# Optimization experiments

Hardware: AMD Instinct MI355X
Metric: run time of the kernel (lower is better)

Reference implementation:

```python
import jax, jax.numpy as jnp
import numpy as np

NUM_HEADS = 16
ROPE_BASE = 10000.0


def _rope_cos_sin(T, head_dim, dtype):
    # standard rotary: angles[t, i] = t * base^(-2i/head_dim), half-split layout
    inv_freq = 1.0 / (ROPE_BASE ** (jnp.arange(0, head_dim, 2, dtype=jnp.float32) / head_dim))
    ang = jnp.arange(T, dtype=jnp.float32)[:, None] * inv_freq[None, :]  # [T, hd/2]
    cos = jnp.concatenate([jnp.cos(ang), jnp.cos(ang)], axis=-1).astype(dtype)  # [T, hd]
    sin = jnp.concatenate([jnp.sin(ang), jnp.sin(ang)], axis=-1).astype(dtype)
    return cos, sin


def _rotate_half(t):
    t1, t2 = jnp.split(t, 2, axis=-1)
    return jnp.concatenate([-t2, t1], axis=-1)


def _apply_rope(t, cos, sin):
    # t: [B, H, T, hd]; cos/sin: [T, hd]
    return t * cos[None, None] + _rotate_half(t) * sin[None, None]


def setup_inputs() -> dict:
    key = jax.random.key(0)
    B, T, C = 2, 2048, 1024
    k1, k2, k3 = jax.random.split(key, 3)
    x = jax.random.normal(k1, (B, T, C), dtype=jnp.float32)
    w_attn = jax.random.normal(k2, (C, 3 * C), dtype=jnp.float32) * (C ** -0.5)
    w_proj = jax.random.normal(k3, (C, C), dtype=jnp.float32) * (C ** -0.5)
    return {"x": x, "w_attn": w_attn, "w_proj": w_proj}


def reference(x, w_attn, w_proj):
    B, T, C = x.shape
    H = NUM_HEADS
    hd = C // H

    qkv = x @ w_attn  # [B, T, 3C]
    q, k, v = jnp.split(qkv, 3, axis=-1)
    # [B, T, C] -> [B, H, T, hd]
    q = q.reshape(B, T, H, hd).transpose(0, 2, 1, 3)
    k = k.reshape(B, T, H, hd).transpose(0, 2, 1, 3)
    v = v.reshape(B, T, H, hd).transpose(0, 2, 1, 3)

    cos, sin = _rope_cos_sin(T, hd, x.dtype)
    q = _apply_rope(q, cos, sin)
    k = _apply_rope(k, cos, sin)

    scale = 1.0 / np.sqrt(hd).astype(np.float32)
    att = jnp.einsum('bhqd,bhkd->bhqk', q, k) * scale  # [B, H, T, T]
    causal = jnp.tril(jnp.ones((T, T), dtype=bool))
    att = jnp.where(causal[None, None], att, jnp.array(-jnp.inf, dtype=att.dtype))
    att = jax.nn.softmax(att, axis=-1)
    y = jnp.einsum('bhqk,bhkd->bhqd', att, v)  # [B, H, T, hd]
    y = y.transpose(0, 2, 1, 3).reshape(B, T, C)
    return y @ w_proj
```

## Files before the change

kernel.cpp:

```cpp
#include <hip/hip_runtime.h>

typedef unsigned short u16;
typedef unsigned int u32;
typedef unsigned long long u64;
typedef __attribute__((ext_vector_type(8))) short s16x8;
typedef __attribute__((ext_vector_type(8))) __bf16 bf16x8;
typedef __attribute__((ext_vector_type(4))) float fx4;
typedef __attribute__((ext_vector_type(16))) float fx16;
typedef __attribute__((ext_vector_type(2))) u32 u32x2;
typedef __attribute__((ext_vector_type(4))) u32 u32x4;

__device__ __forceinline__ fx4 mfma_16x16x32(s16x8 a, s16x8 b, fx4 c) {
  return __builtin_amdgcn_mfma_f32_16x16x32_bf16(
      __builtin_bit_cast(bf16x8, a), __builtin_bit_cast(bf16x8, b), c, 0, 0, 0);
}
__device__ __forceinline__ fx16 mfma_32x32x16(s16x8 a, s16x8 b, fx16 c) {
  return __builtin_amdgcn_mfma_f32_32x32x16_bf16(
      __builtin_bit_cast(bf16x8, a), __builtin_bit_cast(bf16x8, b), c, 0, 0, 0);
}

__device__ __forceinline__ u16 f2bf(float f) {
  u32 u = __builtin_bit_cast(u32, f);
  u32 r = u + 0x7fffu + ((u >> 16) & 1u);
  return (u16)(r >> 16);
}
__device__ __forceinline__ float bf2f(u16 h) {
  u32 u = ((u32)h) << 16;
  return __builtin_bit_cast(float, u);
}

__device__ __forceinline__ u32 cvtpk(float lo, float hi) {
  u32 r;
  asm("v_cvt_pk_bf16_f32 %0, %1, %2" : "=v"(r) : "v"(lo), "v"(hi));
  return r;
}

__device__ __forceinline__ float max3f(float a, float b, float c) {
  float r;
  asm("v_max3_f32 %0, %1, %2, %3" : "=v"(r) : "v"(a), "v"(b), "v"(c));
  return r;
}

__device__ __forceinline__ void plswap(u32& x, u32& y) {
  typedef __attribute__((ext_vector_type(2))) unsigned int uix2;
  uix2 r = __builtin_amdgcn_permlane32_swap(x, y, false, false);
  x = r[0];
  y = r[1];
}

__device__ __forceinline__ float xhalf_max(float v) {
  u32 a = __builtin_bit_cast(u32, v), b = a;
  plswap(a, b);
  return fmaxf(__builtin_bit_cast(float, a), __builtin_bit_cast(float, b));
}
__device__ __forceinline__ float xhalf_sum(float v) {
  u32 a = __builtin_bit_cast(u32, v), b = a;
  plswap(a, b);
  return __builtin_bit_cast(float, a) + __builtin_bit_cast(float, b);
}

__device__ __forceinline__ void gload16(const void* g, void* l) {
  __builtin_amdgcn_global_load_lds(
      (const __attribute__((address_space(1))) u32*)g,
      (__attribute__((address_space(3))) u32*)l, 16, 0, 0);
}

#define B_ 2
#define T_ 2048
#define C_ 1024
#define H_ 16
#define HD_ 64
#define BH_ 32
#define M_ 4096
#define CF_ 0.18033688011112042f

__global__ void rope_table_k(float* __restrict__ ct, float* __restrict__ st) {
  int id = blockIdx.x * 256 + threadIdx.x;
  int t = id >> 5, i = id & 31;
  float f = exp2f(-(float)i * (13.287712379549449f / 32.0f));
  float a = (float)t * f;
  float s, c;
  sincosf(a, &s, &c);
  ct[id] = c;
  st[id] = s;
}

__global__ void cvt_f32_bf16_k(const float* __restrict__ in, u16* __restrict__ outp) {
  int id = blockIdx.x * 256 + threadIdx.x;
  const fx4* p = (const fx4*)(in + (u64)id * 8);
  fx4 v0 = p[0], v1 = p[1];
  s16x8 r;
#pragma unroll
  for (int j = 0; j < 4; ++j) {
    r[j] = (short)f2bf(v0[j]);
    r[4 + j] = (short)f2bf(v1[j]);
  }
  *((s16x8*)outp + id) = r;
}

__global__ void transpose_w_k(const float* __restrict__ W, u16* __restrict__ WT,
                              int Ncols, int R) {
  __shared__ u16 T_s[64 * 72];
  int c0 = blockIdx.x * 64, r0 = blockIdx.y * 64;
  int tid = threadIdx.x;
#pragma unroll
  for (int it = 0; it < 4; ++it) {
    int idx = it * 256 + tid;
    int r = idx >> 4, c4 = (idx & 15) * 4;
    fx4 v = *(const fx4*)(W + (u64)(r0 + r) * Ncols + c0 + c4);
#pragma unroll
    for (int j = 0; j < 4; ++j) T_s[(c4 + j) * 72 + r] = f2bf(v[j]);
  }
  __syncthreads();
#pragma unroll
  for (int it = 0; it < 2; ++it) {
    int idx = it * 256 + tid;
    int rc = idx >> 3, c8 = (idx & 7) * 8;
    s16x8 v = *(const s16x8*)(T_s + rc * 72 + c8);
    *(s16x8*)(WT + (u64)(c0 + rc) * R + r0 + c8) = v;
  }
}

template <int EPI>
__global__ __launch_bounds__(256, 4) void gemm_bt_k(
    const u16* __restrict__ A, const u16* __restrict__ B, float* __restrict__ C,
    u16* __restrict__ Qo, u16* __restrict__ Ko, u16* __restrict__ Vo,
    const float* __restrict__ ct, const float* __restrict__ st,
    int M, int N, int K) {
  __shared__ u16 As[128 * 32];
  __shared__ u16 Bs[128 * 32];
  int tid = threadIdx.x, lane = tid & 63, w = tid >> 6;
  int wm = w >> 1, wn = w & 1, l15 = lane & 15, l4 = lane >> 4;
  int nwg = gridDim.x * gridDim.y;
  int id = blockIdx.y * gridDim.x + blockIdx.x;
  int qq = nwg >> 3;
  id = (id & 7) * qq + (id >> 3);
  int m0 = (id / gridDim.x) * 128, n0 = (id % gridDim.x) * 128;
  fx4 acc[4][4] = {};
  int arow = tid >> 2, ac8 = (tid & 3) * 8;
  const u16* Ab = A + (u64)(m0 + arow) * K + ac8;
  const u16* Bb = B + (u64)(n0 + arow) * K + ac8;
  char* AsB = (char*)As + tid * 16;
  char* BsB = (char*)Bs + tid * 16;

  for (int k0 = 0; k0 < K; k0 += 32) {
    __syncthreads();
    gload16(Ab + k0, AsB);
    gload16(Ab + (u64)64 * K + k0, AsB + 4096);
    gload16(Bb + k0, BsB);
    gload16(Bb + (u64)64 * K + k0, BsB + 4096);
    __syncthreads();
    s16x8 a[4], b[4];
#pragma unroll
    for (int mi = 0; mi < 4; ++mi)
      a[mi] = *(const s16x8*)((const char*)As + (wm * 64 + mi * 16 + l15) * 64 + l4 * 16);
#pragma unroll
    for (int ni = 0; ni < 4; ++ni)
      b[ni] = *(const s16x8*)((const char*)Bs + (wn * 64 + ni * 16 + l15) * 64 + l4 * 16);
#pragma unroll
    for (int mi = 0; mi < 4; ++mi)
#pragma unroll
      for (int ni = 0; ni < 4; ++ni)
        acc[mi][ni] = mfma_16x16x32(a[mi], b[ni], acc[mi][ni]);
  }

  if (EPI == 0) {
#pragma unroll
    for (int mi = 0; mi < 4; ++mi)
#pragma unroll
      for (int ni = 0; ni < 4; ++ni)
#pragma unroll
        for (int r = 0; r < 4; ++r) {
          u64 row = (u64)(m0 + wm * 64 + mi * 16 + l4 * 4 + r);
          int col = n0 + wn * 64 + ni * 16 + l15;
          C[row * N + col] = acc[mi][ni][r];
        }
  } else {
#pragma unroll
    for (int mi = 0; mi < 4; ++mi)
#pragma unroll
      for (int r = 0; r < 4; ++r) {
        int row = m0 + wm * 64 + mi * 16 + l4 * 4 + r;
        int b2 = row >> 11, t = row & (T_ - 1);
#pragma unroll
        for (int ni = 0; ni < 2; ++ni) {
          int col = n0 + wn * 64 + ni * 16 + l15;
          int qi = col >> 10, h = (col >> 6) & 15, d = ni * 16 + l15;
          float lo = acc[mi][ni][r], hi = acc[mi][ni + 2][r];
          if (qi == 2) {
            u64 vbase =
                ((((u64)(b2 * H_ + h)) * (T_ / 8) + (t >> 3)) * HD_ + d) * 8 + (t & 7);
            Vo[vbase] = f2bf(lo);
            Vo[vbase + 32 * 8] = f2bf(hi);
          } else {
            float c = ct[t * 32 + d], s = st[t * 32 + d];
            float sc = (qi == 0) ? CF_ : 1.0f;
            u16* dst = (qi == 0) ? Qo : Ko;
            u64 base = ((((u64)(b2 * H_ + h)) * 8 + (d >> 3)) * T_ + t) * 8 + (d & 7);
            dst[base] = f2bf((lo * c - hi * s) * sc);
            dst[base + (u64)4 * T_ * 8] = f2bf((hi * c + lo * s) * sc);
          }
        }
      }
  }
}


#define LOADK(KC, KVI)                                                 \
  do {                                                                 \
    _Pragma("unroll")                                                  \
    for (int ks_ = 0; ks_ < 4; ++ks_)                                  \
      KC[ks_] = *(const s16x8*)(kp[ks_] + (u64)(KVI) * 256);           \
  } while (0)

#define LOADV(VC, KVI)                                                 \
  do {                                                                 \
    const u16* vk_ = vpb + (u64)(KVI) * 2048;                          \
    VC[0] = *(const s16x8*)(vk_);                                      \
    VC[1] = *(const s16x8*)(vk_ + 256);                                \
    VC[2] = *(const s16x8*)(vk_ + 1024);                               \
    VC[3] = *(const s16x8*)(vk_ + 1280);                               \
  } while (0)

#define ATTN_STEP(KC, VC, KVI)                                                \
  do {                                                                        \
    fx16 s_ = {};                                                             \
    __builtin_amdgcn_s_setprio(1);                                            \
    _Pragma("unroll")                                                         \
    for (int ks_ = 0; ks_ < 4; ++ks_)                                         \
      s_ = mfma_32x32x16(KC[ks_], qf[ks_], s_);                               \
    __builtin_amdgcn_s_setprio(0);                                            \
    if ((KVI) == jt) {                                                        \
      _Pragma("unroll")                                                       \
      for (int r_ = 0; r_ < 16; ++r_) {                                       \
        int cr_ = (r_ & 3) + 8 * (r_ >> 2) + 4 * h;                           \
        s_[r_] = (cr_ > ql) ? -1e30f : s_[r_];                                \
      }                                                                       \
    }                                                                         \
    float u0_ = max3f(s_[0], s_[1], s_[2]);                                   \
    float u1_ = max3f(s_[3], s_[4], s_[5]);                                   \
    float u2_ = max3f(s_[6], s_[7], s_[8]);                                   \
    float u3_ = max3f(s_[9], s_[10], s_[11]);                                 \
    float u4_ = max3f(s_[12], s_[13], s_[14]);                                \
    float v0_ = max3f(u0_, u1_, s_[15]);                                      \
    float v1_ = max3f(u2_, u3_, u4_);                                         \
    float rowmax_ = xhalf_max(fmaxf(v0_, v1_));                               \
    if (!__all(rowmax_ <= m + 8.f)) {                                         \
      float mnew_ = fmaxf(m, rowmax_);                                        \
      float corr_ = exp2f(m - mnew_);                                         \
      l *= corr_;                                                             \
      oL *= corr_;                                                            \
      oH *= corr_;                                                            \
      m = mnew_;                                                              \
    }                                                                         \
    float p_[16];                                                             \
    _Pragma("unroll")                                                         \
    for (int r_ = 0; r_ < 16; ++r_) p_[r_] = exp2f(s_[r_] - m);               \
    float a0_ = (p_[0] + p_[8]) + (p_[1] + p_[9]);                            \
    float a1_ = (p_[2] + p_[10]) + (p_[3] + p_[11]);                          \
    float a2_ = (p_[4] + p_[12]) + (p_[5] + p_[13]);                          \
    float a3_ = (p_[6] + p_[14]) + (p_[7] + p_[15]);                          \
    l += xhalf_sum((a0_ + a1_) + (a2_ + a3_));                                \
    u32 x0_ = cvtpk(p_[0], p_[1]), x1_ = cvtpk(p_[2], p_[3]);                 \
    u32 y0_ = cvtpk(p_[4], p_[5]), y1_ = cvtpk(p_[6], p_[7]);                 \
    plswap(x0_, y0_);                                                         \
    plswap(x1_, y1_);                                                         \
    u32x4 f0w_ = {x0_, x1_, y0_, y1_};                                        \
    u32 x2_ = cvtpk(p_[8], p_[9]), x3_ = cvtpk(p_[10], p_[11]);               \
    u32 y2_ = cvtpk(p_[12], p_[13]), y3_ = cvtpk(p_[14], p_[15]);             \
    plswap(x2_, y2_);                                                         \
    plswap(x3_, y3_);                                                         \
    u32x4 f1w_ = {x2_, x3_, y2_, y3_};                                        \
    s16x8 pf0_ = __builtin_bit_cast(s16x8, f0w_);                             \
    s16x8 pf1_ = __builtin_bit_cast(s16x8, f1w_);                             \
    __builtin_amdgcn_s_setprio(1);                                            \
    oL = mfma_32x32x16(VC[0], pf0_, oL);                                      \
    oH = mfma_32x32x16(VC[1], pf0_, oH);                                      \
    oL = mfma_32x32x16(VC[2], pf1_, oL);                                      \
    oH = mfma_32x32x16(VC[3], pf1_, oH);                                      \
    __builtin_amdgcn_s_setprio(0);                                            \
  } while (0)

#define OSTRIDE 68

__global__ __launch_bounds__(256, 3) void attn_fwd_k(
    const u16* __restrict__ Qp, const u16* __restrict__ Kp,
    const u16* __restrict__ Vp, u16* __restrict__ Y) {
  __shared__ float Ob[4 * 32 * OSTRIDE];
  __shared__ float Ml[4 * 32 * 2];
  int tid = threadIdx.x, lane = tid & 63, w = tid >> 6;
  int ql = lane & 31, h = lane >> 5;
  int bh = blockIdx.x & 31;
  int jt = 63 - (blockIdx.x >> 5);
  int q0 = jt * 32;
  int b2 = bh >> 4, head = bh & 15;
  int n = jt + 1;
  int lo = (w * n) >> 2, hi = ((w + 1) * n) >> 2;

  s16x8 qf[4];
#pragma unroll
  for (int ks = 0; ks < 4; ++ks)
    qf[ks] = *(const s16x8*)(Qp + (((u64)bh * 8 + ks * 2 + h) * T_ + q0 + ql) * 8);

  const u16* kp[4];
#pragma unroll
  for (int ks = 0; ks < 4; ++ks)
    kp[ks] = Kp + (((u64)bh * 8 + ks * 2 + h) * T_ + ql) * 8;
  const u16* vpb = Vp + (((u64)bh * (T_ / 8) + h) * HD_ + ql) * 8;

  fx16 oL = {}, oH = {};
  float m = -1e30f, l = 0.f;

  if (lo < hi) {
    s16x8 kA[4], vA[4], kB[4], vB[4];
    LOADK(kA, lo);
    LOADV(vA, lo);
    int kv = lo;
    for (; kv + 1 < hi; kv += 2) {
      LOADK(kB, kv + 1);
      LOADV(vB, kv + 1);
      ATTN_STEP(kA, vA, kv);
      if (kv + 2 < hi) {
        LOADK(kA, kv + 2);
        LOADV(vA, kv + 2);
      }
      ATTN_STEP(kB, vB, kv + 1);
    }
    if (kv < hi) ATTN_STEP(kA, vA, kv);
  }

  {
    float* ob = Ob + (w * 32 + ql) * OSTRIDE;
#pragma unroll
    for (int g = 0; g < 4; ++g) {
      fx4 a = {oL[4 * g], oL[4 * g + 1], oL[4 * g + 2], oL[4 * g + 3]};
      *(fx4*)(ob + 8 * g + 4 * h) = a;
      fx4 b = {oH[4 * g], oH[4 * g + 1], oH[4 * g + 2], oH[4 * g + 3]};
      *(fx4*)(ob + 32 + 8 * g + 4 * h) = b;
    }
    if (h == 0) {
      Ml[(w * 32 + ql) * 2] = m;
      Ml[(w * 32 + ql) * 2 + 1] = l;
    }
  }
  __syncthreads();

  {
    int q = tid >> 3, db = tid & 7;
    float mm0 = Ml[(0 * 32 + q) * 2], ll0 = Ml[(0 * 32 + q) * 2 + 1];
    float mm1 = Ml[(1 * 32 + q) * 2], ll1 = Ml[(1 * 32 + q) * 2 + 1];
    float mm2 = Ml[(2 * 32 + q) * 2], ll2 = Ml[(2 * 32 + q) * 2 + 1];
    float mm3 = Ml[(3 * 32 + q) * 2], ll3 = Ml[(3 * 32 + q) * 2 + 1];
    float mo = fmaxf(fmaxf(mm0, mm1), fmaxf(mm2, mm3));
    float w0 = exp2f(mm0 - mo), w1 = exp2f(mm1 - mo);
    float w2 = exp2f(mm2 - mo), w3 = exp2f(mm3 - mo);
    float rl = 1.0f / (ll0 * w0 + ll1 * w1 + ll2 * w2 + ll3 * w3);
    w0 *= rl; w1 *= rl; w2 *= rl; w3 *= rl;
    const float* ob = Ob + q * OSTRIDE + db * 8;
    fx4 aa = {}, bb = {};
#pragma unroll
    for (int i = 0; i < 4; ++i) {
      float wi = (i == 0) ? w0 : (i == 1) ? w1 : (i == 2) ? w2 : w3;
      fx4 pa = *(const fx4*)(ob + i * 32 * OSTRIDE);
      fx4 pb = *(const fx4*)(ob + i * 32 * OSTRIDE + 4);
      aa += wi * pa;
      bb += wi * pb;
    }
    u32x4 ow;
    ow[0] = cvtpk(aa[0], aa[1]);
    ow[1] = cvtpk(aa[2], aa[3]);
    ow[2] = cvtpk(bb[0], bb[1]);
    ow[3] = cvtpk(bb[2], bb[3]);
    int t = q0 + q;
    *(u32x4*)(Y + ((u64)(b2 * T_ + t)) * C_ + head * HD_ + db * 8) = ow;
  }
}

extern "C" void kernel_launch(void* const* d_in, const int* in_sizes, int n_in,
                              void* d_out, int out_size, void* d_ws, size_t ws_size,
                              hipStream_t stream) {
  (void)in_sizes; (void)n_in; (void)out_size; (void)ws_size;
  const float* x = (const float*)d_in[0];
  const float* w_attn = (const float*)d_in[1];
  const float* w_proj = (const float*)d_in[2];
  float* out = (float*)d_out;

  u16* xb = (u16*)d_ws;
  u16* waT = xb + (u64)M_ * C_;
  u16* wpT = waT + (u64)3 * C_ * C_;
  u16* Qp = wpT + (u64)C_ * C_;
  u16* Kp = Qp + (u64)BH_ * T_ * HD_;
  u16* Vp = Kp + (u64)BH_ * T_ * HD_;
  float* ct = (float*)(Vp + (u64)BH_ * T_ * HD_);
  float* st = ct + T_ * 32;
  u16* yb = xb;

  rope_table_k<<<256, 256, 0, stream>>>(ct, st);
  cvt_f32_bf16_k<<<(M_ * C_ / 8) / 256, 256, 0, stream>>>(x, xb);
  transpose_w_k<<<dim3(48, 16), 256, 0, stream>>>(w_attn, waT, 3 * C_, C_);
  transpose_w_k<<<dim3(16, 16), 256, 0, stream>>>(w_proj, wpT, C_, C_);

  gemm_bt_k<1><<<dim3(24, 32), 256, 0, stream>>>(xb, waT, nullptr, Qp, Kp, Vp,
                                                 ct, st, M_, 3 * C_, C_);

  attn_fwd_k<<<2048, 256, 0, stream>>>(Qp, Kp, Vp, yb);

  gemm_bt_k<0><<<dim3(8, 32), 256, 0, stream>>>(yb, wpT, out, nullptr, nullptr,
                                                nullptr, nullptr, nullptr,
                                                M_, C_, C_);
}
```

Before: 121.0 us.

## Triple-buffer GEMM LDS loads with swizzle and merge prep kernels into one launch

Rewrites the GEMM main loop to use a three-stage LDS ring buffer with asynchronous global-to-LDS loads issued two tiles ahead. Explicit vmcnt waits replace the full load/sync per k-step, so memory latency overlaps with MFMA work. An XOR swizzle on LDS slots aims to reduce bank conflicts. The four preprocessing kernels (rope table, x conversion, two weight transposes) are fused into one launch to cut launch overhead. The larger LDS footprint lowers launch_bounds occupancy from 4 to 3 blocks per SM.

```diff
diff --git a/kernel.cpp b/kernel.cpp
--- a/kernel.cpp
+++ b/kernel.cpp
@@ -74,61 +74,71 @@
 #define M_ 4096
 #define CF_ 0.18033688011112042f
 
-__global__ void rope_table_k(float* __restrict__ ct, float* __restrict__ st) {
-  int id = blockIdx.x * 256 + threadIdx.x;
-  int t = id >> 5, i = id & 31;
-  float f = exp2f(-(float)i * (13.287712379549449f / 32.0f));
-  float a = (float)t * f;
-  float s, c;
-  sincosf(a, &s, &c);
-  ct[id] = c;
-  st[id] = s;
-}
-
-__global__ void cvt_f32_bf16_k(const float* __restrict__ in, u16* __restrict__ outp) {
-  int id = blockIdx.x * 256 + threadIdx.x;
-  const fx4* p = (const fx4*)(in + (u64)id * 8);
-  fx4 v0 = p[0], v1 = p[1];
-  s16x8 r;
-#pragma unroll
-  for (int j = 0; j < 4; ++j) {
-    r[j] = (short)f2bf(v0[j]);
-    r[4 + j] = (short)f2bf(v1[j]);
-  }
-  *((s16x8*)outp + id) = r;
-}
-
-__global__ void transpose_w_k(const float* __restrict__ W, u16* __restrict__ WT,
-                              int Ncols, int R) {
+__global__ __launch_bounds__(256) void prep_k(
+    const float* __restrict__ x, const float* __restrict__ wa,
+    const float* __restrict__ wp, u16* __restrict__ xb, u16* __restrict__ waT,
+    u16* __restrict__ wpT, float* __restrict__ ct, float* __restrict__ st) {
   __shared__ u16 T_s[64 * 72];
-  int c0 = blockIdx.x * 64, r0 = blockIdx.y * 64;
-  int tid = threadIdx.x;
-#pragma unroll
-  for (int it = 0; it < 4; ++it) {
-    int idx = it * 256 + tid;
-    int r = idx >> 4, c4 = (idx & 15) * 4;
-    fx4 v = *(const fx4*)(W + (u64)(r0 + r) * Ncols + c0 + c4);
-#pragma unroll
-    for (int j = 0; j < 4; ++j) T_s[(c4 + j) * 72 + r] = f2bf(v[j]);
-  }
-  __syncthreads();
-#pragma unroll
-  for (int it = 0; it < 2; ++it) {
-    int idx = it * 256 + tid;
-    int rc = idx >> 3, c8 = (idx & 7) * 8;
-    s16x8 v = *(const s16x8*)(T_s + rc * 72 + c8);
-    *(s16x8*)(WT + (u64)(c0 + rc) * R + r0 + c8) = v;
+  int b = blockIdx.x, tid = threadIdx.x;
+  if (b < 2048) {
+    int id = b * 256 + tid;
+    const fx4* p = (const fx4*)(x + (u64)id * 8);
+    fx4 v0 = p[0], v1 = p[1];
+    s16x8 r;
+#pragma unroll
+    for (int j = 0; j < 4; ++j) {
+      r[j] = (short)f2bf(v0[j]);
+      r[4 + j] = (short)f2bf(v1[j]);
+    }
+    *((s16x8*)xb + id) = r;
+  } else if (b < 3072) {
+    const float* W;
+    u16* WT;
+    int Ncols, bx, by;
+    if (b < 2816) {
+      int i = b - 2048;
+      W = wa; WT = waT; Ncols = 3072; bx = i % 48; by = i / 48;
+    } else {
+      int i = b - 2816;
+      W = wp; WT = wpT; Ncols = 1024; bx = i % 16; by = i / 16;
+    }
+    int c0 = bx * 64, r0 = by * 64;
+#pragma unroll
+    for (int it = 0; it < 4; ++it) {
+      int idx = it * 256 + tid;
+      int r = idx >> 4, c4 = (idx & 15) * 4;
+      fx4 v = *(const fx4*)(W + (u64)(r0 + r) * Ncols + c0 + c4);
+#pragma unroll
+      for (int j = 0; j < 4; ++j) T_s[(c4 + j) * 72 + r] = f2bf(v[j]);
+    }
+    __syncthreads();
+#pragma unroll
+    for (int it = 0; it < 2; ++it) {
+      int idx = it * 256 + tid;
+      int rc = idx >> 3, c8 = (idx & 7) * 8;
+      s16x8 v = *(const s16x8*)(T_s + rc * 72 + c8);
+      *(s16x8*)(WT + (u64)(c0 + rc) * 1024 + r0 + c8) = v;
+    }
+  } else {
+    int id = (b - 3072) * 256 + tid;
+    int t = id >> 5, i = id & 31;
+    float f = exp2f(-(float)i * (13.287712379549449f / 32.0f));
+    float a = (float)t * f;
+    float s, c;
+    sincosf(a, &s, &c);
+    ct[id] = c;
+    st[id] = s;
   }
 }
 
 template <int EPI>
-__global__ __launch_bounds__(256, 4) void gemm_bt_k(
+__global__ __launch_bounds__(256, 3) void gemm_bt_k(
     const u16* __restrict__ A, const u16* __restrict__ B, float* __restrict__ C,
     u16* __restrict__ Qo, u16* __restrict__ Ko, u16* __restrict__ Vo,
     const float* __restrict__ ct, const float* __restrict__ st,
     int M, int N, int K) {
-  __shared__ u16 As[128 * 32];
-  __shared__ u16 Bs[128 * 32];
+  __shared__ u16 AsS[3][128 * 32];
+  __shared__ u16 BsS[3][128 * 32];
   int tid = threadIdx.x, lane = tid & 63, w = tid >> 6;
   int wm = w >> 1, wn = w & 1, l15 = lane & 15, l4 = lane >> 4;
   int nwg = gridDim.x * gridDim.y;
@@ -137,32 +147,73 @@
   id = (id & 7) * qq + (id >> 3);
   int m0 = (id / gridDim.x) * 128, n0 = (id % gridDim.x) * 128;
   fx4 acc[4][4] = {};
-  int arow = tid >> 2, ac8 = (tid & 3) * 8;
-  const u16* Ab = A + (u64)(m0 + arow) * K + ac8;
-  const u16* Bb = B + (u64)(n0 + arow) * K + ac8;
-  char* AsB = (char*)As + tid * 16;
-  char* BsB = (char*)Bs + tid * 16;
-
-  for (int k0 = 0; k0 < K; k0 += 32) {
-    __syncthreads();
-    gload16(Ab + k0, AsB);
-    gload16(Ab + (u64)64 * K + k0, AsB + 4096);
-    gload16(Bb + k0, BsB);
-    gload16(Bb + (u64)64 * K + k0, BsB + 4096);
-    __syncthreads();
-    s16x8 a[4], b[4];
-#pragma unroll
-    for (int mi = 0; mi < 4; ++mi)
-      a[mi] = *(const s16x8*)((const char*)As + (wm * 64 + mi * 16 + l15) * 64 + l4 * 16);
-#pragma unroll
-    for (int ni = 0; ni < 4; ++ni)
-      b[ni] = *(const s16x8*)((const char*)Bs + (wn * 64 + ni * 16 + l15) * 64 + l4 * 16);
-#pragma unroll
-    for (int mi = 0; mi < 4; ++mi)
-#pragma unroll
-      for (int ni = 0; ni < 4; ++ni)
-        acc[mi][ni] = mfma_16x16x32(a[mi], b[ni], acc[mi][ni]);
-  }
+
+  const u16* asrc[2];
+  const u16* bsrc[2];
+#pragma unroll
+  for (int g = 0; g < 2; ++g) {
+    int idx = g * 256 + tid;
+    int row = idx >> 2, slot = (idx & 3) ^ (row & 3);
+    asrc[g] = A + (u64)(m0 + row) * K + slot * 8;
+    bsrc[g] = B + (u64)(n0 + row) * K + slot * 8;
+  }
+
+#define GSTAGE(S, KOFF)                                                      \
+  do {                                                                       \
+    _Pragma("unroll")                                                        \
+    for (int g_ = 0; g_ < 2; ++g_) {                                         \
+      gload16(asrc[g_] + (KOFF), (char*)AsS[S] + g_ * 4096 + tid * 16);      \
+      gload16(bsrc[g_] + (KOFF), (char*)BsS[S] + g_ * 4096 + tid * 16);      \
+    }                                                                        \
+  } while (0)
+
+#define GCOMP(S)                                                             \
+  do {                                                                       \
+    s16x8 a_[4], b_[4];                                                      \
+    _Pragma("unroll")                                                        \
+    for (int mi_ = 0; mi_ < 4; ++mi_) {                                      \
+      int r_ = wm * 64 + mi_ * 16 + l15;                                     \
+      a_[mi_] = *(const s16x8*)((const char*)AsS[S] + r_ * 64 +              \
+                                ((l4 ^ (r_ & 3)) * 16));                     \
+    }                                                                        \
+    _Pragma("unroll")                                                        \
+    for (int ni_ = 0; ni_ < 4; ++ni_) {                                      \
+      int r_ = wn * 64 + ni_ * 16 + l15;                                     \
+      b_[ni_] = *(const s16x8*)((const char*)BsS[S] + r_ * 64 +              \
+                                ((l4 ^ (r_ & 3)) * 16));                     \
+    }                                                                        \
+    _Pragma("unroll")                                                        \
+    for (int mi_ = 0; mi_ < 4; ++mi_)                                        \
+      _Pragma("unroll")                                                      \
+      for (int ni_ = 0; ni_ < 4; ++ni_)                                      \
+        acc[mi_][ni_] = mfma_16x16x32(a_[mi_], b_[ni_], acc[mi_][ni_]);      \
+  } while (0)
+
+  int NT = K >> 5;
+  GSTAGE(0, 0);
+  GSTAGE(1, 32);
+  int s0 = 0, s1 = 1, s2 = 2;
+  for (int t = 0; t < NT; ++t) {
+    __builtin_amdgcn_s_barrier();
+    __builtin_amdgcn_sched_barrier(0);
+    if (t + 2 < NT) GSTAGE(s2, (t + 2) * 32);
+    __builtin_amdgcn_sched_barrier(0);
+    if (t < NT - 2)
+      asm volatile("s_waitcnt vmcnt(8)" ::: "memory");
+    else if (t == NT - 2)
+      asm volatile("s_waitcnt vmcnt(4)" ::: "memory");
+    else
+      asm volatile("s_waitcnt vmcnt(0)" ::: "memory");
+    __builtin_amdgcn_s_barrier();
+    __builtin_amdgcn_sched_barrier(0);
+    GCOMP(s0);
+    int tmp = s0;
+    s0 = s1;
+    s1 = s2;
+    s2 = tmp;
+  }
+#undef GSTAGE
+#undef GCOMP
 
   if (EPI == 0) {
 #pragma unroll
@@ -395,10 +446,7 @@
   float* st = ct + T_ * 32;
   u16* yb = xb;
 
-  rope_table_k<<<256, 256, 0, stream>>>(ct, st);
-  cvt_f32_bf16_k<<<(M_ * C_ / 8) / 256, 256, 0, stream>>>(x, xb);
-  transpose_w_k<<<dim3(48, 16), 256, 0, stream>>>(w_attn, waT, 3 * C_, C_);
-  transpose_w_k<<<dim3(16, 16), 256, 0, stream>>>(w_proj, wpT, C_, C_);
+  prep_k<<<3328, 256, 0, stream>>>(x, w_attn, w_proj, xb, waT, wpT, ct, st);
 
   gemm_bt_k<1><<<dim3(24, 32), 256, 0, stream>>>(xb, waT, nullptr, Qp, Kp, Vp,
                                                  ct, st, M_, 3 * C_, C_);
```

New measurement: 111.7 us. 1.08x faster.
